# Performance work log

Hardware: AMD Instinct MI355X
Metric: run time of the kernel (lower is better)

## Reference

```python
import jax, jax.numpy as jnp
import numpy as np

# Dimensions
B, LQ, HQ, HKV, D = 4, 512, 16, 8, 128          # seqs, q tokens/seq, q heads, kv heads, head dim
BLOCK_SIZE, BLOCKS_PER_SEQ, NUM_BLOCKS = 256, 8, 64  # paged KV-cache geometry
CTX = BLOCK_SIZE * BLOCKS_PER_SEQ                # cached tokens per seq (full blocks, rem=0)
LK = CTX + LQ                                    # keys per seq = cache + current step
DIFF_BLOCK = 128                                 # diffusion block: bidirectional inside, causal across
SCALE = 1.0 / float(np.sqrt(D))


def _make_allow_mask():
    # True = allowed to attend. All cached tokens visible; within the current
    # step, query attends up to the end of its own diffusion block (block-causal,
    # intra-block bidirectional) -- the semantics described in the module docstring.
    qi = jnp.arange(LQ)
    kj = jnp.arange(LK)
    limit = CTX + ((qi // DIFF_BLOCK) + 1) * DIFF_BLOCK   # [LQ]
    m = kj[None, :] < limit[:, None]                      # [LQ, LK]
    return jnp.broadcast_to(m[None], (B, LQ, LK))


def setup_inputs() -> dict:
    key = jax.random.key(0)
    ks = jax.random.split(key, 6)
    q = jax.random.normal(ks[0], (B, LQ, HQ, D), jnp.float32)
    k = jax.random.normal(ks[1], (B, LQ, HKV, D), jnp.float32)
    v = jax.random.normal(ks[2], (B, LQ, HKV, D), jnp.float32)
    k_cache = jax.random.normal(ks[3], (NUM_BLOCKS, BLOCK_SIZE, HKV, D), jnp.float32)
    v_cache = jax.random.normal(ks[4], (NUM_BLOCKS, BLOCK_SIZE, HKV, D), jnp.float32)
    # distinct physical block slots per sequence (as a paged allocator would give)
    block_tables = jax.random.permutation(ks[5], NUM_BLOCKS)[: B * BLOCKS_PER_SEQ]
    block_tables = block_tables.reshape(B, BLOCKS_PER_SEQ).astype(jnp.int32)
    allow_mask = _make_allow_mask()
    return dict(q=q, k=k, v=v, k_cache=k_cache, v_cache=v_cache,
                block_tables=block_tables, allow_mask=allow_mask)


def reference(q, k, v, k_cache, v_cache, block_tables, allow_mask):
    rep = HQ // HKV
    # paged gather: [B, nblk, blk, Hkv, D] -> [B, CTX, Hkv, D]
    K_ctx = k_cache[block_tables].reshape(B, CTX, HKV, D)
    V_ctx = v_cache[block_tables].reshape(B, CTX, HKV, D)
    K_all = jnp.concatenate([K_ctx, k], axis=1)   # [B, LK, Hkv, D]
    V_all = jnp.concatenate([V_ctx, v], axis=1)
    # GQA: repeat_interleave kv heads to q heads
    K_all = jnp.repeat(K_all, rep, axis=2)        # [B, LK, Hq, D]
    V_all = jnp.repeat(V_all, rep, axis=2)
    scores = jnp.einsum('bqhd,bkhd->bhqk', q * SCALE, K_all)  # [B, Hq, LQ, LK]
    neg = jnp.finfo(scores.dtype).min
    scores = jnp.where(allow_mask[:, None, :, :], scores, neg)
    attn = jax.nn.softmax(scores, axis=-1)
    return jnp.einsum('bhqk,bkhd->bqhd', attn, V_all)         # [B, LQ, Hq, D]
```

## Files before the change

kernel.cpp:

```cpp
#include <hip/hip_runtime.h>
#include <hip/hip_bf16.h>


#define B_    4
#define LQ_   512
#define HQ_   16
#define HKV_  8
#define D_    128
#define BLKSZ_ 256
#define BPS_  8
#define CTX_  2048
#define DIFFB_ 128
#define KT_   64
#define SCALE_ 0.08838834764831845f

typedef __attribute__((ext_vector_type(4))) float f32x4;
typedef __attribute__((ext_vector_type(8))) short bf16x8;

__device__ __forceinline__ unsigned cvt_pk2(float a, float b) {
  union { __hip_bfloat162 h; unsigned u; } x;
  x.h = __float22bfloat162_rn(float2{a, b});
  return x.u;
}
union bf8u { bf16x8 v; unsigned u[4]; };

__device__ __forceinline__ int kidx(int kv, int d) {
  return kv * 128 + ((((d >> 3) ^ kv) & 15) << 3) + (d & 7);
}
__device__ __forceinline__ int vidx(int d, int p) {
  return d * 64 + ((((p >> 3) ^ d ^ (d >> 3)) & 7) << 3) + (p & 7);
}
__device__ __forceinline__ int pk32(int w) {
  return (((w >> 2) & 3) << 3) | (((w >> 4) & 1) << 2) | (w & 3);
}

__global__ __launch_bounds__(1024)
void block_attn_kernel(const float* __restrict__ qg,
                       const float* __restrict__ kcur,
                       const float* __restrict__ vcur,
                       const float* __restrict__ kcache,
                       const float* __restrict__ vcache,
                       const int*   __restrict__ btab,
                       float*       __restrict__ out) {
  const int blk  = blockIdx.x;
  const int hkv  = blk & 7;
  const int b    = (blk >> 3) & 3;
  const int qb   = blk >> 5;
  const int tid  = threadIdx.x;
  const int lane = tid & 63;
  const int wave = tid >> 6;
  const int lo   = lane & 15;
  const int hi   = lane >> 4;
  const int g2   = wave >> 1;
  const int kvh  = wave & 1;
  const int hq   = hkv * 2 + (g2 >> 2);
  const int qrow0 = qb * 64 + (g2 & 3) * 16;
  const int limit  = CTX_ + (qb / 2 + 1) * DIFFB_;
  const int ntiles = limit / KT_;

  __shared__ __align__(16) char smem_raw[65536];
  __shared__ float ms[8][16], ls[8][16];
  float* Os = (float*)smem_raw;

  bf16x8 qf[4];
  {
    const float* qr = qg + ((size_t)((b * LQ_ + qrow0 + lo)) * HQ_ + hq) * D_;
#pragma unroll
    for (int db = 0; db < 4; ++db) {
      const int d0 = db * 32 + hi * 8;
      f32x4 a = *(const f32x4*)(qr + d0);
      f32x4 c4 = *(const f32x4*)(qr + d0 + 4);
      bf8u f;
      f.u[0] = cvt_pk2(a[0] * SCALE_, a[1] * SCALE_);
      f.u[1] = cvt_pk2(a[2] * SCALE_, a[3] * SCALE_);
      f.u[2] = cvt_pk2(c4[0] * SCALE_, c4[1] * SCALE_);
      f.u[3] = cvt_pk2(c4[2] * SCALE_, c4[3] * SCALE_);
      qf[db] = f.v;
    }
  }

  f32x4 oacc[8];
#pragma unroll
  for (int i = 0; i < 8; ++i) oacc[i] = (f32x4){0.f, 0.f, 0.f, 0.f};
  float mrow = -1e30f, lrow = 0.f;

  const int c  = tid >> 4;
  const int e  = tid & 15;
  const int r0 = c & ~1;
  const int ep = (c & 1) * 16 + e;
  const int pr = (r0 & 32) + pk32(r0 & 31);
  f32x4 kreg[2], vreg[2];

  auto issue_loads = [&](int t) {
    const int kbase = t * KT_;
    const float *kr, *vr0;
    if (kbase < CTX_) {
      const int pb = btab[b * BPS_ + (kbase >> 8)];
      const int ro = (kbase & 255);
      kr  = kcache + ((size_t)(pb * BLKSZ_ + ro + c)  * HKV_ + hkv) * D_;
      vr0 = vcache + ((size_t)(pb * BLKSZ_ + ro + r0) * HKV_ + hkv) * D_;
    } else {
      const int cur = kbase - CTX_;
      kr  = kcur + ((size_t)(b * LQ_ + cur + c)  * HKV_ + hkv) * D_;
      vr0 = vcur + ((size_t)(b * LQ_ + cur + r0) * HKV_ + hkv) * D_;
    }
    const int kd0 = e * 8;
    kreg[0] = *(const f32x4*)(kr + kd0);
    kreg[1] = *(const f32x4*)(kr + kd0 + 4);
    const int vd0 = ep * 4;
    vreg[0] = *(const f32x4*)(vr0 + vd0);
    vreg[1] = *(const f32x4*)(vr0 + HKV_ * D_ + vd0);
  };

  auto write_lds = [&](int bsel) {
    short* Kb = (short*)(smem_raw + bsel * 16384);
    short* Vb = (short*)(smem_raw + 32768 + bsel * 16384);
    const int kd0 = e * 8;
    *(unsigned*)&Kb[kidx(c, kd0)]     = cvt_pk2(kreg[0][0], kreg[0][1]);
    *(unsigned*)&Kb[kidx(c, kd0 + 2)] = cvt_pk2(kreg[0][2], kreg[0][3]);
    *(unsigned*)&Kb[kidx(c, kd0 + 4)] = cvt_pk2(kreg[1][0], kreg[1][1]);
    *(unsigned*)&Kb[kidx(c, kd0 + 6)] = cvt_pk2(kreg[1][2], kreg[1][3]);
    const int vd0 = ep * 4;
#pragma unroll
    for (int j = 0; j < 4; ++j)
      *(unsigned*)&Vb[vidx(vd0 + j, pr)] = cvt_pk2(vreg[0][j], vreg[1][j]);
  };

  issue_loads(0);
  write_lds(0);
  __syncthreads();

  for (int t = 0; t < ntiles; ++t) {
    const int bsel = t & 1;
    const short* Kb = (const short*)(smem_raw + bsel * 16384);
    const short* Vb = (const short*)(smem_raw + 32768 + bsel * 16384);
    if (t + 1 < ntiles) issue_loads(t + 1);

    f32x4 sacc[2];
    sacc[0] = (f32x4){0.f, 0.f, 0.f, 0.f};
    sacc[1] = (f32x4){0.f, 0.f, 0.f, 0.f};
#pragma unroll
    for (int cs = 0; cs < 2; ++cs)
#pragma unroll
      for (int db = 0; db < 4; ++db) {
        bf16x8 kf = *(const bf16x8*)&Kb[kidx(kvh * 32 + cs * 16 + lo,
                                             db * 32 + hi * 8)];
        sacc[cs] = __builtin_amdgcn_mfma_f32_16x16x32_bf16(kf, qf[db], sacc[cs], 0, 0, 0);
      }

    float mx;
    {
      float m0 = fmaxf(fmaxf(sacc[0][0], sacc[0][1]), fmaxf(sacc[0][2], sacc[0][3]));
      float m1 = fmaxf(fmaxf(sacc[1][0], sacc[1][1]), fmaxf(sacc[1][2], sacc[1][3]));
      mx = fmaxf(m0, m1);
      mx = fmaxf(mx, __shfl_xor(mx, 16));
      mx = fmaxf(mx, __shfl_xor(mx, 32));
    }
    const bool keep = __all(mx - mrow <= 8.0f);
    const float mnew = keep ? mrow : fmaxf(mrow, mx);
    float rs = 0.f;
#pragma unroll
    for (int cs = 0; cs < 2; ++cs)
#pragma unroll
      for (int i = 0; i < 4; ++i) {
        const float p = __expf(sacc[cs][i] - mnew);
        sacc[cs][i] = p;
        rs += p;
      }
    rs += __shfl_xor(rs, 16);
    rs += __shfl_xor(rs, 32);
    if (keep) {
      lrow += rs;
    } else {
      const float sc = __expf(mrow - mnew);
      lrow = lrow * sc + rs;
      mrow = mnew;
#pragma unroll
      for (int dt = 0; dt < 8; ++dt) oacc[dt] *= sc;
    }

    bf16x8 pa;
    {
      bf8u p;
      p.u[0] = cvt_pk2(sacc[0][0], sacc[0][1]);
      p.u[1] = cvt_pk2(sacc[0][2], sacc[0][3]);
      p.u[2] = cvt_pk2(sacc[1][0], sacc[1][1]);
      p.u[3] = cvt_pk2(sacc[1][2], sacc[1][3]);
      pa = p.v;
    }

#pragma unroll
    for (int dt = 0; dt < 8; ++dt) {
      bf16x8 vf = *(const bf16x8*)&Vb[vidx(dt * 16 + lo, kvh * 32 + hi * 8)];
      oacc[dt] = __builtin_amdgcn_mfma_f32_16x16x32_bf16(vf, pa, oacc[dt], 0, 0, 0);
    }

    if (t + 1 < ntiles) write_lds(bsel ^ 1);
    __syncthreads();
  }

  if (kvh == 1) {
#pragma unroll
    for (int dt = 0; dt < 8; ++dt)
      *(f32x4*)&Os[(size_t)(g2 * 16 + lo) * 128 + dt * 16 + hi * 4] = oacc[dt];
    if (hi == 0) { ms[g2][lo] = mrow; ls[g2][lo] = lrow; }
  }
  __syncthreads();
  if (kvh == 0) {
    const float m1 = ms[g2][lo], l1 = ls[g2][lo];
    const float mstar = fmaxf(mrow, m1);
    const float a0 = __expf(mrow - mstar);
    const float a1 = __expf(m1 - mstar);
    const float linv = 1.f / (lrow * a0 + l1 * a1);
    float* orow = out + ((size_t)(b * LQ_ + qrow0 + lo) * HQ_ + hq) * D_;
#pragma unroll
    for (int dt = 0; dt < 8; ++dt) {
      f32x4 o1 = *(const f32x4*)&Os[(size_t)(g2 * 16 + lo) * 128 + dt * 16 + hi * 4];
      f32x4 o = (oacc[dt] * a0 + o1 * a1) * linv;
      *(f32x4*)(orow + dt * 16 + hi * 4) = o;
    }
  }
}

extern "C" void kernel_launch(void* const* d_in, const int* in_sizes, int n_in,
                              void* d_out, int out_size, void* d_ws, size_t ws_size,
                              hipStream_t stream) {
  (void)in_sizes; (void)n_in; (void)out_size; (void)d_ws; (void)ws_size;
  const float* q      = (const float*)d_in[0];
  const float* k      = (const float*)d_in[1];
  const float* v      = (const float*)d_in[2];
  const float* kcache = (const float*)d_in[3];
  const float* vcache = (const float*)d_in[4];
  const int*   btab   = (const int*)d_in[5];
  float* out = (float*)d_out;

  block_attn_kernel<<<dim3(B_ * HKV_ * (LQ_ / 64)), dim3(1024), 0, stream>>>(
      q, k, v, kcache, vcache, btab, out);
}
```

Baseline: 87.13 us.

## Pair early and late query blocks per workgroup to balance causal work

Each workgroup now serves two 32-row query chunks, one from the front and its mirror from the back of the sequence, so every block does a similar amount of causal work. All tiles up to a fixed maximum are loaded into shared memory, and each wave skips compute on tiles beyond its own diffusion-block limit. Global-load assignments for K and V are reorganised for wider coalesced reads and 64-bit LDS stores. The cost is that waves with shorter limits sit idle through the barriers, and the grid decomposition is unchanged.

```diff
diff --git a/kernel.cpp b/kernel.cpp
--- a/kernel.cpp
+++ b/kernel.cpp
@@ -12,10 +12,12 @@
 #define CTX_  2048
 #define DIFFB_ 128
 #define KT_   64
+#define NTMAX_ 40
 #define SCALE_ 0.08838834764831845f
 
 typedef __attribute__((ext_vector_type(4))) float f32x4;
 typedef __attribute__((ext_vector_type(8))) short bf16x8;
+typedef __attribute__((ext_vector_type(2))) unsigned u32x2;
 
 __device__ __forceinline__ unsigned cvt_pk2(float a, float b) {
   union { __hip_bfloat162 h; unsigned u; } x;
@@ -45,18 +47,20 @@
   const int blk  = blockIdx.x;
   const int hkv  = blk & 7;
   const int b    = (blk >> 3) & 3;
-  const int qb   = blk >> 5;
+  const int qp   = blk >> 5;
   const int tid  = threadIdx.x;
   const int lane = tid & 63;
   const int wave = tid >> 6;
   const int lo   = lane & 15;
   const int hi   = lane >> 4;
+  const int qsel = wave >> 3;
+  const int qb32 = qsel ? (15 - qp) : qp;
+  const int g2l  = (wave >> 1) & 3;
+  const int kvh  = wave & 1;
   const int g2   = wave >> 1;
-  const int kvh  = wave & 1;
-  const int hq   = hkv * 2 + (g2 >> 2);
-  const int qrow0 = qb * 64 + (g2 & 3) * 16;
-  const int limit  = CTX_ + (qb / 2 + 1) * DIFFB_;
-  const int ntiles = limit / KT_;
+  const int hq   = hkv * 2 + (g2l >> 1);
+  const int qrow0 = qb32 * 32 + (g2l & 1) * 16;
+  const int ntw  = 34 + 2 * (qb32 >> 2);
 
   __shared__ __align__(16) char smem_raw[65536];
   __shared__ float ms[8][16], ls[8][16];
@@ -84,118 +88,124 @@
   for (int i = 0; i < 8; ++i) oacc[i] = (f32x4){0.f, 0.f, 0.f, 0.f};
   float mrow = -1e30f, lrow = 0.f;
 
-  const int c  = tid >> 4;
-  const int e  = tid & 15;
-  const int r0 = c & ~1;
-  const int ep = (c & 1) * 16 + e;
-  const int pr = (r0 & 32) + pk32(r0 & 31);
+  const int l31  = lane & 31;
+  const int rK0  = 2 * wave + (lane >> 5);
+  const int gq   = lane >> 4;
+  const int ev   = lane & 15;
+  const int vr0  = 32 * (wave >> 3) + 16 * (gq >> 1) + 4 * (wave & 3) + 2 * (gq & 1);
+  const int vD0  = 64 * ((wave >> 2) & 1) + 4 * ev;
+  const int vpr  = (vr0 & 32) + pk32(vr0 & 31);
   f32x4 kreg[2], vreg[2];
 
   auto issue_loads = [&](int t) {
     const int kbase = t * KT_;
-    const float *kr, *vr0;
+    const float *kb_, *vb_;
     if (kbase < CTX_) {
       const int pb = btab[b * BPS_ + (kbase >> 8)];
-      const int ro = (kbase & 255);
-      kr  = kcache + ((size_t)(pb * BLKSZ_ + ro + c)  * HKV_ + hkv) * D_;
-      vr0 = vcache + ((size_t)(pb * BLKSZ_ + ro + r0) * HKV_ + hkv) * D_;
+      const int ro = kbase & 255;
+      const size_t base = ((size_t)(pb * BLKSZ_ + ro) * HKV_ + hkv) * D_;
+      kb_ = kcache + base;
+      vb_ = vcache + base;
     } else {
       const int cur = kbase - CTX_;
-      kr  = kcur + ((size_t)(b * LQ_ + cur + c)  * HKV_ + hkv) * D_;
-      vr0 = vcur + ((size_t)(b * LQ_ + cur + r0) * HKV_ + hkv) * D_;
-    }
-    const int kd0 = e * 8;
-    kreg[0] = *(const f32x4*)(kr + kd0);
-    kreg[1] = *(const f32x4*)(kr + kd0 + 4);
-    const int vd0 = ep * 4;
-    vreg[0] = *(const f32x4*)(vr0 + vd0);
-    vreg[1] = *(const f32x4*)(vr0 + HKV_ * D_ + vd0);
+      const size_t base = ((size_t)(b * LQ_ + cur) * HKV_ + hkv) * D_;
+      kb_ = kcur + base;
+      vb_ = vcur + base;
+    }
+    const size_t rs = (size_t)HKV_ * D_;
+    kreg[0] = *(const f32x4*)(kb_ + (size_t)rK0 * rs + 4 * l31);
+    kreg[1] = *(const f32x4*)(kb_ + (size_t)(rK0 + 32) * rs + 4 * l31);
+    vreg[0] = *(const f32x4*)(vb_ + (size_t)vr0 * rs + vD0);
+    vreg[1] = *(const f32x4*)(vb_ + (size_t)(vr0 + 1) * rs + vD0);
   };
 
   auto write_lds = [&](int bsel) {
     short* Kb = (short*)(smem_raw + bsel * 16384);
     short* Vb = (short*)(smem_raw + 32768 + bsel * 16384);
-    const int kd0 = e * 8;
-    *(unsigned*)&Kb[kidx(c, kd0)]     = cvt_pk2(kreg[0][0], kreg[0][1]);
-    *(unsigned*)&Kb[kidx(c, kd0 + 2)] = cvt_pk2(kreg[0][2], kreg[0][3]);
-    *(unsigned*)&Kb[kidx(c, kd0 + 4)] = cvt_pk2(kreg[1][0], kreg[1][1]);
-    *(unsigned*)&Kb[kidx(c, kd0 + 6)] = cvt_pk2(kreg[1][2], kreg[1][3]);
-    const int vd0 = ep * 4;
+#pragma unroll
+    for (int i = 0; i < 2; ++i) {
+      u32x2 w;
+      w[0] = cvt_pk2(kreg[i][0], kreg[i][1]);
+      w[1] = cvt_pk2(kreg[i][2], kreg[i][3]);
+      *(u32x2*)&Kb[kidx(rK0 + 32 * i, 4 * l31)] = w;
+    }
 #pragma unroll
     for (int j = 0; j < 4; ++j)
-      *(unsigned*)&Vb[vidx(vd0 + j, pr)] = cvt_pk2(vreg[0][j], vreg[1][j]);
+      *(unsigned*)&Vb[vidx(vD0 + j, vpr)] = cvt_pk2(vreg[0][j], vreg[1][j]);
   };
 
   issue_loads(0);
   write_lds(0);
   __syncthreads();
 
-  for (int t = 0; t < ntiles; ++t) {
+  for (int t = 0; t < NTMAX_; ++t) {
     const int bsel = t & 1;
     const short* Kb = (const short*)(smem_raw + bsel * 16384);
     const short* Vb = (const short*)(smem_raw + 32768 + bsel * 16384);
-    if (t + 1 < ntiles) issue_loads(t + 1);
-
-    f32x4 sacc[2];
-    sacc[0] = (f32x4){0.f, 0.f, 0.f, 0.f};
-    sacc[1] = (f32x4){0.f, 0.f, 0.f, 0.f};
-#pragma unroll
-    for (int cs = 0; cs < 2; ++cs)
-#pragma unroll
-      for (int db = 0; db < 4; ++db) {
-        bf16x8 kf = *(const bf16x8*)&Kb[kidx(kvh * 32 + cs * 16 + lo,
-                                             db * 32 + hi * 8)];
-        sacc[cs] = __builtin_amdgcn_mfma_f32_16x16x32_bf16(kf, qf[db], sacc[cs], 0, 0, 0);
-      }
-
-    float mx;
-    {
-      float m0 = fmaxf(fmaxf(sacc[0][0], sacc[0][1]), fmaxf(sacc[0][2], sacc[0][3]));
-      float m1 = fmaxf(fmaxf(sacc[1][0], sacc[1][1]), fmaxf(sacc[1][2], sacc[1][3]));
-      mx = fmaxf(m0, m1);
-      mx = fmaxf(mx, __shfl_xor(mx, 16));
-      mx = fmaxf(mx, __shfl_xor(mx, 32));
-    }
-    const bool keep = __all(mx - mrow <= 8.0f);
-    const float mnew = keep ? mrow : fmaxf(mrow, mx);
-    float rs = 0.f;
-#pragma unroll
-    for (int cs = 0; cs < 2; ++cs)
-#pragma unroll
-      for (int i = 0; i < 4; ++i) {
-        const float p = __expf(sacc[cs][i] - mnew);
-        sacc[cs][i] = p;
-        rs += p;
-      }
-    rs += __shfl_xor(rs, 16);
-    rs += __shfl_xor(rs, 32);
-    if (keep) {
-      lrow += rs;
-    } else {
-      const float sc = __expf(mrow - mnew);
-      lrow = lrow * sc + rs;
-      mrow = mnew;
-#pragma unroll
-      for (int dt = 0; dt < 8; ++dt) oacc[dt] *= sc;
-    }
-
-    bf16x8 pa;
-    {
-      bf8u p;
-      p.u[0] = cvt_pk2(sacc[0][0], sacc[0][1]);
-      p.u[1] = cvt_pk2(sacc[0][2], sacc[0][3]);
-      p.u[2] = cvt_pk2(sacc[1][0], sacc[1][1]);
-      p.u[3] = cvt_pk2(sacc[1][2], sacc[1][3]);
-      pa = p.v;
-    }
-
-#pragma unroll
-    for (int dt = 0; dt < 8; ++dt) {
-      bf16x8 vf = *(const bf16x8*)&Vb[vidx(dt * 16 + lo, kvh * 32 + hi * 8)];
-      oacc[dt] = __builtin_amdgcn_mfma_f32_16x16x32_bf16(vf, pa, oacc[dt], 0, 0, 0);
-    }
-
-    if (t + 1 < ntiles) write_lds(bsel ^ 1);
+    if (t + 1 < NTMAX_) issue_loads(t + 1);
+
+    if (t < ntw) {
+      f32x4 sacc[2];
+      sacc[0] = (f32x4){0.f, 0.f, 0.f, 0.f};
+      sacc[1] = (f32x4){0.f, 0.f, 0.f, 0.f};
+#pragma unroll
+      for (int cs = 0; cs < 2; ++cs)
+#pragma unroll
+        for (int db = 0; db < 4; ++db) {
+          bf16x8 kf = *(const bf16x8*)&Kb[kidx(kvh * 32 + cs * 16 + lo,
+                                               db * 32 + hi * 8)];
+          sacc[cs] = __builtin_amdgcn_mfma_f32_16x16x32_bf16(kf, qf[db], sacc[cs], 0, 0, 0);
+        }
+
+      float mx;
+      {
+        float m0 = fmaxf(fmaxf(sacc[0][0], sacc[0][1]), fmaxf(sacc[0][2], sacc[0][3]));
+        float m1 = fmaxf(fmaxf(sacc[1][0], sacc[1][1]), fmaxf(sacc[1][2], sacc[1][3]));
+        mx = fmaxf(m0, m1);
+        mx = fmaxf(mx, __shfl_xor(mx, 16));
+        mx = fmaxf(mx, __shfl_xor(mx, 32));
+      }
+      const bool keep = __all(mx - mrow <= 8.0f);
+      const float mnew = keep ? mrow : fmaxf(mrow, mx);
+      float rs = 0.f;
+#pragma unroll
+      for (int cs = 0; cs < 2; ++cs)
+#pragma unroll
+        for (int i = 0; i < 4; ++i) {
+          const float pv = __expf(sacc[cs][i] - mnew);
+          sacc[cs][i] = pv;
+          rs += pv;
+        }
+      rs += __shfl_xor(rs, 16);
+      rs += __shfl_xor(rs, 32);
+      if (keep) {
+        lrow += rs;
+      } else {
+        const float sc = __expf(mrow - mnew);
+        lrow = lrow * sc + rs;
+        mrow = mnew;
+#pragma unroll
+        for (int dt = 0; dt < 8; ++dt) oacc[dt] *= sc;
+      }
+
+      bf16x8 pa;
+      {
+        bf8u pk;
+        pk.u[0] = cvt_pk2(sacc[0][0], sacc[0][1]);
+        pk.u[1] = cvt_pk2(sacc[0][2], sacc[0][3]);
+        pk.u[2] = cvt_pk2(sacc[1][0], sacc[1][1]);
+        pk.u[3] = cvt_pk2(sacc[1][2], sacc[1][3]);
+        pa = pk.v;
+      }
+
+#pragma unroll
+      for (int dt = 0; dt < 8; ++dt) {
+        bf16x8 vf = *(const bf16x8*)&Vb[vidx(dt * 16 + lo, kvh * 32 + hi * 8)];
+        oacc[dt] = __builtin_amdgcn_mfma_f32_16x16x32_bf16(vf, pa, oacc[dt], 0, 0, 0);
+      }
+    }
+
+    if (t + 1 < NTMAX_) write_lds(bsel ^ 1);
     __syncthreads();
   }
 
```

Result: slower. 88.95 us (+2.1%).
